# Optimization experiments

Measured on AMD Instinct MI355X. Metric: run time of the kernel, lower is better.

## Reference

```python
import jax, jax.numpy as jnp
import numpy as np

MARGIN = 0.3

def _cdist(x):
    # pairwise euclidean distances, safe sqrt (zero grad at 0)
    sq = jnp.sum(x * x, axis=1)
    d2 = sq[:, None] + sq[None, :] - 2.0 * (x @ x.T)
    d2 = jnp.maximum(d2, 0.0)
    safe = jnp.where(d2 > 0, d2, 1.0)
    return jnp.where(d2 > 0, jnp.sqrt(safe), 0.0)

def setup_inputs() -> dict:
    key = jax.random.key(0)
    k1, k2 = jax.random.split(key)
    embeddings = jax.random.normal(k1, (4096, 128), dtype=jnp.float32)
    labels = jax.random.randint(k2, (4096,), 0, 256)
    return {"embeddings": embeddings, "labels": labels}

def reference(embeddings, labels):
    B = embeddings.shape[0]
    dist = _cdist(embeddings)                      # [B, B]
    same = labels[:, None] == labels[None, :]      # [B, B]
    eye = jnp.eye(B, dtype=bool)
    pos_mask = same & ~eye
    neg_mask = ~same
    neg_inf = jnp.array(-jnp.inf, dist.dtype)
    pos_inf = jnp.array(jnp.inf, dist.dtype)
    hard_pos = jnp.max(jnp.where(pos_mask, dist, neg_inf), axis=1)  # [B]
    hard_neg = jnp.min(jnp.where(neg_mask, dist, pos_inf), axis=1)  # [B]
    valid = jnp.any(pos_mask, axis=1) & jnp.any(neg_mask, axis=1)
    per_row = jax.nn.relu(hard_pos - hard_neg + MARGIN)
    per_row = jnp.where(valid, per_row, 0.0)
    num_valid = jnp.sum(valid.astype(dist.dtype))
    return jnp.sum(per_row) / jnp.maximum(num_valid, 1.0)
```

## Files before the change

kernel.cpp:

```cpp
#include <hip/hip_runtime.h>
#include <hip/hip_bf16.h>


typedef __attribute__((ext_vector_type(8))) short short8;
typedef __attribute__((ext_vector_type(4))) float f32x4;

#define MARGIN_F 0.3f
#define NEG_BIG -3.4e38f
#define POS_BIG 3.4e38f
#define WAITVM(N) __builtin_amdgcn_s_waitcnt(((N)&15)|((((N)>>4)&3)<<14)|(7<<4)|(15<<8))

__device__ __forceinline__ void gl_lds16(const void* g, void* l) {
    __builtin_amdgcn_global_load_lds(
        (const __attribute__((address_space(1))) void*)g,
        (__attribute__((address_space(3))) void*)l, 16, 0, 0);
}

__device__ inline unsigned short f2bf(float x) {
    union { __hip_bfloat16 h; unsigned short u; } c;
    c.h = __float2bfloat16(x);
    return c.u;
}

__global__ __launch_bounds__(256) void tl_prep(const float* __restrict__ E,
                                               unsigned short* __restrict__ Ebf,
                                               float* __restrict__ sqn,
                                               unsigned* __restrict__ cnt) {
    int t = blockIdx.x * 256 + threadIdx.x;
    if (t < 4) cnt[t] = 0u;
    int row = t >> 5;
    int kq = (t & 31) * 4;
    float4 v = *(const float4*)&E[(size_t)row * 128 + kq];
    float s = fmaf(v.x, v.x, fmaf(v.y, v.y, fmaf(v.z, v.z, v.w * v.w)));
    ushort4 h4;
    h4.x = f2bf(v.x); h4.y = f2bf(v.y); h4.z = f2bf(v.z); h4.w = f2bf(v.w);
    *(ushort4*)&Ebf[(size_t)row * 128 + kq] = h4;
#pragma unroll
    for (int m = 1; m < 32; m <<= 1) s += __shfl_xor(s, m);
    if ((t & 31) == 0) sqn[row] = s;
}

__global__ __launch_bounds__(256, 4) void tl_phase1(const unsigned short* __restrict__ Ebf,
                                                    const int* __restrict__ labels,
                                                    const float* __restrict__ sqn,
                                                    float* __restrict__ pmp,
                                                    float* __restrict__ pmn) {
    union SM {
        unsigned short B[2][128 * 64];
        struct { float mp[128][32]; float mn[128][32]; } f;
    };
    __shared__ __align__(16) SM sm;

    const int tid = threadIdx.x;
    const int l = tid & 63, w = tid >> 6;
    const int wr = w >> 1, wc = w & 1;
    const int q = l >> 4, r16 = l & 15;
    const int i0 = blockIdx.x * 128, j0 = blockIdx.y * 128;

    const unsigned short* gB[4];
#pragma unroll
    for (int t2 = 0; t2 < 4; ++t2) {
        int s = w * 256 + t2 * 64 + l;
        int row = s >> 3, ch = (s & 7) ^ (row & 7);
        gB[t2] = Ebf + (size_t)(j0 + row) * 128 + ch * 8;
    }
#pragma unroll
    for (int t2 = 0; t2 < 4; ++t2)
        gl_lds16(gB[t2], &sm.B[0][w * 2048 + t2 * 512]);
#pragma unroll
    for (int t2 = 0; t2 < 4; ++t2)
        gl_lds16(gB[t2] + 64, &sm.B[1][w * 2048 + t2 * 512]);

    int li[4][4], lj[4];
    float sj[4];
#pragma unroll
    for (int ti = 0; ti < 4; ++ti)
#pragma unroll
        for (int p = 0; p < 4; ++p)
            li[ti][p] = labels[i0 + wr * 64 + ti * 16 + q * 4 + p];
#pragma unroll
    for (int tj = 0; tj < 4; ++tj) {
        int cj = j0 + wc * 64 + tj * 16 + r16;
        lj[tj] = labels[cj];
        sj[tj] = sqn[cj];
    }

    const unsigned short* aBase = Ebf + (size_t)(i0 + wr * 64 + r16) * 128 + q * 8;

    f32x4 acc[4][4];
#pragma unroll
    for (int ti = 0; ti < 4; ++ti)
#pragma unroll
        for (int tj = 0; tj < 4; ++tj) acc[ti][tj] = (f32x4)0.0f;

#pragma unroll
    for (int kc = 0; kc < 2; ++kc) {
        if (kc == 0) WAITVM(4); else WAITVM(0);
        __builtin_amdgcn_s_barrier();
#pragma unroll
        for (int s = 0; s < 2; ++s) {
            short8 af[4], bf[4];
            const int cA = ((s * 4 + q) ^ (r16 & 7)) * 8;
#pragma unroll
            for (int t2 = 0; t2 < 4; ++t2) {
                af[t2] = *(const short8*)(aBase + (size_t)t2 * 16 * 128 + kc * 64 + s * 32);
                bf[t2] = *(const short8*)&sm.B[kc][(wc * 64 + t2 * 16 + r16) * 64 + cA];
            }
#pragma unroll
            for (int ti = 0; ti < 4; ++ti)
#pragma unroll
                for (int tj = 0; tj < 4; ++tj)
                    acc[ti][tj] = __builtin_amdgcn_mfma_f32_16x16x32_bf16(
                        af[ti], bf[tj], acc[ti][tj], 0, 0, 0);
        }
    }

    float mp[4][4], mn[4][4];
#pragma unroll
    for (int ti = 0; ti < 4; ++ti)
#pragma unroll
        for (int p = 0; p < 4; ++p) { mp[ti][p] = NEG_BIG; mn[ti][p] = POS_BIG; }
    const bool diagblk = (blockIdx.x == blockIdx.y);
#pragma unroll
    for (int tj = 0; tj < 4; ++tj) {
#pragma unroll
        for (int ti = 0; ti < 4; ++ti)
#pragma unroll
            for (int p = 0; p < 4; ++p) {
                float val = fmaf(-2.0f, acc[ti][tj][p], sj[tj]);
                bool same = (li[ti][p] == lj[tj]);
                bool self = diagblk &&
                    ((wr * 64 + ti * 16 + q * 4 + p) == (wc * 64 + tj * 16 + r16));
                mp[ti][p] = fmaxf(mp[ti][p], (same && !self) ? val : NEG_BIG);
                mn[ti][p] = fminf(mn[ti][p], same ? POS_BIG : val);
            }
    }

    __syncthreads();
#pragma unroll
    for (int ti = 0; ti < 4; ++ti)
#pragma unroll
        for (int p = 0; p < 4; ++p) {
            int rloc = wr * 64 + ti * 16 + q * 4 + p;
            sm.f.mp[rloc][wc * 16 + r16] = mp[ti][p];
            sm.f.mn[rloc][wc * 16 + r16] = mn[ti][p];
        }
    __syncthreads();
    if (tid < 128) {
        const float4* P = (const float4*)&sm.f.mp[tid][0];
        const float4* N = (const float4*)&sm.f.mn[tid][0];
        float M = NEG_BIG, m_ = POS_BIG;
#pragma unroll
        for (int k = 0; k < 8; ++k) {
            float4 p4 = P[k], n4 = N[k];
            M = fmaxf(M, fmaxf(fmaxf(p4.x, p4.y), fmaxf(p4.z, p4.w)));
            m_ = fminf(m_, fminf(fminf(n4.x, n4.y), fminf(n4.z, n4.w)));
        }
        pmp[(size_t)blockIdx.y * 4096 + i0 + tid] = M;
        pmn[(size_t)blockIdx.y * 4096 + i0 + tid] = m_;
    }
}

__global__ __launch_bounds__(256) void tl_phase2(const float* __restrict__ pmp,
                                                 const float* __restrict__ pmn,
                                                 const float* __restrict__ sqn,
                                                 unsigned* __restrict__ cnt,
                                                 float* __restrict__ accum,
                                                 float* __restrict__ out) {
    __shared__ float sp[4], sv[4];
    int tid = threadIdx.x;
    int r = blockIdx.x * 256 + tid;
    float mp = NEG_BIG, mn = POS_BIG;
#pragma unroll
    for (int k = 0; k < 32; ++k) {
        mp = fmaxf(mp, pmp[(size_t)k * 4096 + r]);
        mn = fminf(mn, pmn[(size_t)k * 4096 + r]);
    }
    float si = sqn[r];
    bool valid = (mp > 0.5f * NEG_BIG) && (mn < 0.5f * POS_BIG);
    float hp = sqrtf(fmaxf(si + mp, 0.0f));
    float hn = sqrtf(fmaxf(si + mn, 0.0f));
    float pr = fmaxf(hp - hn + MARGIN_F, 0.0f);
    float s = valid ? pr : 0.0f;
    float n = valid ? 1.0f : 0.0f;
#pragma unroll
    for (int m = 1; m < 64; m <<= 1) {
        s += __shfl_xor(s, m);
        n += __shfl_xor(n, m);
    }
    if ((tid & 63) == 0) { sp[tid >> 6] = s; sv[tid >> 6] = n; }
    __syncthreads();
    if (tid == 0) {
        atomicAdd(&accum[0], sp[0] + sp[1] + sp[2] + sp[3]);
        atomicAdd(&accum[1], sv[0] + sv[1] + sv[2] + sv[3]);
        __threadfence();
        unsigned tk = atomicAdd(&cnt[2], 1u);
        if (tk == 15u) {
            float a = atomicAdd(&accum[0], 0.0f);
            float b = atomicAdd(&accum[1], 0.0f);
            out[0] = a / fmaxf(b, 1.0f);
        }
    }
}

extern "C" void kernel_launch(void* const* d_in, const int* in_sizes, int n_in,
                              void* d_out, int out_size, void* d_ws, size_t ws_size,
                              hipStream_t stream) {
    const float* E = (const float*)d_in[0];
    const int* labels = (const int*)d_in[1];
    float* out = (float*)d_out;

    char* base = (char*)d_ws;
    unsigned short* Ebf = (unsigned short*)base;
    float* pmp = (float*)(base + (1u << 20));
    float* pmn = (float*)(base + (1u << 20) + (512u << 10));
    float* sqn = (float*)(base + (2u << 20));
    unsigned* cnt = (unsigned*)(base + (2u << 20) + (16u << 10));
    float* accum = (float*)(cnt + 8);

    tl_prep<<<512, 256, 0, stream>>>(E, Ebf, sqn, cnt);
    tl_phase1<<<dim3(32, 32), 256, 0, stream>>>(Ebf, labels, sqn, pmp, pmn);
    tl_phase2<<<16, 256, 0, stream>>>(pmp, pmn, sqn, cnt, accum, out);
}
```

Measured before the change: 85.08 us.

## Drop LDS staging: load B fragments directly from global, reduce partials via shuffles

The phase-1 kernel no longer stages the B tile into LDS with async global-to-LDS loads and barriers. Both A and B MFMA fragments are now read straight from global memory (L2-resident bf16). The cross-column max/min reduction now uses wavefront shuffles instead of an LDS transpose with two block syncs. Each wave-column writes its own partial plane, which doubles the partial buffers and the phase-2 reduction loop. This removes barriers and LDS traffic and frees occupancy, at the cost of more global and L2 reads and more partial-result writes.

```diff
diff --git a/kernel.cpp b/kernel.cpp
--- a/kernel.cpp
+++ b/kernel.cpp
@@ -8,13 +8,6 @@
 #define MARGIN_F 0.3f
 #define NEG_BIG -3.4e38f
 #define POS_BIG 3.4e38f
-#define WAITVM(N) __builtin_amdgcn_s_waitcnt(((N)&15)|((((N)>>4)&3)<<14)|(7<<4)|(15<<8))
-
-__device__ __forceinline__ void gl_lds16(const void* g, void* l) {
-    __builtin_amdgcn_global_load_lds(
-        (const __attribute__((address_space(1))) void*)g,
-        (__attribute__((address_space(3))) void*)l, 16, 0, 0);
-}
 
 __device__ inline unsigned short f2bf(float x) {
     union { __hip_bfloat16 h; unsigned short u; } c;
@@ -40,36 +33,19 @@
     if ((t & 31) == 0) sqn[row] = s;
 }
 
-__global__ __launch_bounds__(256, 4) void tl_phase1(const unsigned short* __restrict__ Ebf,
-                                                    const int* __restrict__ labels,
-                                                    const float* __restrict__ sqn,
-                                                    float* __restrict__ pmp,
-                                                    float* __restrict__ pmn) {
-    union SM {
-        unsigned short B[2][128 * 64];
-        struct { float mp[128][32]; float mn[128][32]; } f;
-    };
-    __shared__ __align__(16) SM sm;
-
+__global__ __launch_bounds__(256) void tl_phase1(const unsigned short* __restrict__ Ebf,
+                                                 const int* __restrict__ labels,
+                                                 const float* __restrict__ sqn,
+                                                 float* __restrict__ pmp,
+                                                 float* __restrict__ pmn) {
     const int tid = threadIdx.x;
     const int l = tid & 63, w = tid >> 6;
     const int wr = w >> 1, wc = w & 1;
     const int q = l >> 4, r16 = l & 15;
     const int i0 = blockIdx.x * 128, j0 = blockIdx.y * 128;
 
-    const unsigned short* gB[4];
-#pragma unroll
-    for (int t2 = 0; t2 < 4; ++t2) {
-        int s = w * 256 + t2 * 64 + l;
-        int row = s >> 3, ch = (s & 7) ^ (row & 7);
-        gB[t2] = Ebf + (size_t)(j0 + row) * 128 + ch * 8;
-    }
-#pragma unroll
-    for (int t2 = 0; t2 < 4; ++t2)
-        gl_lds16(gB[t2], &sm.B[0][w * 2048 + t2 * 512]);
-#pragma unroll
-    for (int t2 = 0; t2 < 4; ++t2)
-        gl_lds16(gB[t2] + 64, &sm.B[1][w * 2048 + t2 * 512]);
+    const unsigned short* aB = Ebf + (size_t)(i0 + wr * 64 + r16) * 128 + q * 8;
+    const unsigned short* bB = Ebf + (size_t)(j0 + wc * 64 + r16) * 128 + q * 8;
 
     int li[4][4], lj[4];
     float sj[4];
@@ -85,8 +61,6 @@
         sj[tj] = sqn[cj];
     }
 
-    const unsigned short* aBase = Ebf + (size_t)(i0 + wr * 64 + r16) * 128 + q * 8;
-
     f32x4 acc[4][4];
 #pragma unroll
     for (int ti = 0; ti < 4; ++ti)
@@ -95,24 +69,22 @@
 
 #pragma unroll
     for (int kc = 0; kc < 2; ++kc) {
-        if (kc == 0) WAITVM(4); else WAITVM(0);
-        __builtin_amdgcn_s_barrier();
+        short8 af[4][2], bf8[4][2];
 #pragma unroll
-        for (int s = 0; s < 2; ++s) {
-            short8 af[4], bf[4];
-            const int cA = ((s * 4 + q) ^ (r16 & 7)) * 8;
+        for (int t2 = 0; t2 < 4; ++t2)
 #pragma unroll
-            for (int t2 = 0; t2 < 4; ++t2) {
-                af[t2] = *(const short8*)(aBase + (size_t)t2 * 16 * 128 + kc * 64 + s * 32);
-                bf[t2] = *(const short8*)&sm.B[kc][(wc * 64 + t2 * 16 + r16) * 64 + cA];
+            for (int s = 0; s < 2; ++s) {
+                af[t2][s] = *(const short8*)(aB + (size_t)t2 * 16 * 128 + kc * 64 + s * 32);
+                bf8[t2][s] = *(const short8*)(bB + (size_t)t2 * 16 * 128 + kc * 64 + s * 32);
             }
+#pragma unroll
+        for (int s = 0; s < 2; ++s)
 #pragma unroll
             for (int ti = 0; ti < 4; ++ti)
 #pragma unroll
                 for (int tj = 0; tj < 4; ++tj)
                     acc[ti][tj] = __builtin_amdgcn_mfma_f32_16x16x32_bf16(
-                        af[ti], bf[tj], acc[ti][tj], 0, 0, 0);
-        }
+                        af[ti][s], bf8[tj][s], acc[ti][tj], 0, 0, 0);
     }
 
     float mp[4][4], mn[4][4];
@@ -136,29 +108,23 @@
             }
     }
 
-    __syncthreads();
+    const int plane = blockIdx.y * 2 + wc;
 #pragma unroll
     for (int ti = 0; ti < 4; ++ti)
 #pragma unroll
         for (int p = 0; p < 4; ++p) {
-            int rloc = wr * 64 + ti * 16 + q * 4 + p;
-            sm.f.mp[rloc][wc * 16 + r16] = mp[ti][p];
-            sm.f.mn[rloc][wc * 16 + r16] = mn[ti][p];
+            float a = mp[ti][p], b = mn[ti][p];
+#pragma unroll
+            for (int m = 1; m < 16; m <<= 1) {
+                a = fmaxf(a, __shfl_xor(a, m));
+                b = fminf(b, __shfl_xor(b, m));
+            }
+            if (r16 == 0) {
+                int rrow = i0 + wr * 64 + ti * 16 + q * 4 + p;
+                pmp[(size_t)plane * 4096 + rrow] = a;
+                pmn[(size_t)plane * 4096 + rrow] = b;
+            }
         }
-    __syncthreads();
-    if (tid < 128) {
-        const float4* P = (const float4*)&sm.f.mp[tid][0];
-        const float4* N = (const float4*)&sm.f.mn[tid][0];
-        float M = NEG_BIG, m_ = POS_BIG;
-#pragma unroll
-        for (int k = 0; k < 8; ++k) {
-            float4 p4 = P[k], n4 = N[k];
-            M = fmaxf(M, fmaxf(fmaxf(p4.x, p4.y), fmaxf(p4.z, p4.w)));
-            m_ = fminf(m_, fminf(fminf(n4.x, n4.y), fminf(n4.z, n4.w)));
-        }
-        pmp[(size_t)blockIdx.y * 4096 + i0 + tid] = M;
-        pmn[(size_t)blockIdx.y * 4096 + i0 + tid] = m_;
-    }
 }
 
 __global__ __launch_bounds__(256) void tl_phase2(const float* __restrict__ pmp,
@@ -172,7 +138,7 @@
     int r = blockIdx.x * 256 + tid;
     float mp = NEG_BIG, mn = POS_BIG;
 #pragma unroll
-    for (int k = 0; k < 32; ++k) {
+    for (int k = 0; k < 64; ++k) {
         mp = fmaxf(mp, pmp[(size_t)k * 4096 + r]);
         mn = fminf(mn, pmn[(size_t)k * 4096 + r]);
     }
@@ -213,9 +179,9 @@
     char* base = (char*)d_ws;
     unsigned short* Ebf = (unsigned short*)base;
     float* pmp = (float*)(base + (1u << 20));
-    float* pmn = (float*)(base + (1u << 20) + (512u << 10));
-    float* sqn = (float*)(base + (2u << 20));
-    unsigned* cnt = (unsigned*)(base + (2u << 20) + (16u << 10));
+    float* pmn = (float*)(base + (2u << 20));
+    float* sqn = (float*)(base + (3u << 20));
+    unsigned* cnt = (unsigned*)(base + (3u << 20) + (16u << 10));
     float* accum = (float*)(cnt + 8);
 
     tl_prep<<<512, 256, 0, stream>>>(E, Ebf, sqn, cnt);
```

Result: slower. 102.6 us (+20.6%).
